# Kernel tuning notes

Hardware: AMD Instinct MI355X
Metric: run time of the kernel (lower is better)

Reference implementation:

```python
import jax, jax.numpy as jnp
import numpy as np

T = 16777216  # series length (2**24)


def setup_inputs() -> dict:
    key = jax.random.key(0)
    k1, k2 = jax.random.split(key)
    timeseries = jax.random.normal(k1, (T,), dtype=jnp.float32)
    # learned smoothing parameter alpha in (0, 1), per min_max_norm(0, 1) constraint
    alpha = jax.random.uniform(k2, (1,), dtype=jnp.float32)
    return {"timeseries": timeseries, "alpha": alpha}


def reference(timeseries, alpha):
    """Simple exponential smoothing (component form).

    level_0 = y_0; level_t = (1-alpha)*level_{t-1} + alpha*y_t for t >= 1.
    prediction_t (the forecast emitted at step t) is the level BEFORE the
    update, so the output is levels[0 : T-1], length T-1 (matches the
    original loop that emits one forecast per timestep in timeseries[1:]).

    Expressed as a first-order linear recurrence s_t = a_t * s_{t-1} + b_t
    and solved with an associative (parallel) scan.
    """
    a0 = alpha[0]
    n = timeseries.shape[0]
    dt = timeseries.dtype
    # a_0 = 0, b_0 = y_0 pins level_0 = y_0 regardless of the dummy carry.
    a = jnp.concatenate([jnp.zeros((1,), dt),
                         jnp.full((n - 1,), 1.0, dt) * (1.0 - a0)])
    b = jnp.concatenate([timeseries[:1], a0 * timeseries[1:]])

    def combine(e1, e2):
        a1, b1 = e1
        a2, b2 = e2
        return (a1 * a2, a2 * b1 + b2)

    _, levels = jax.lax.associative_scan(combine, (a, b))  # levels[t] = level_t
    return levels[:-1]
```

## Files before the change

kernel.cpp:

```cpp
#include <hip/hip_runtime.h>
#include <stdint.h>


#define BLOCK 256
#define SEG   32
#define VPT   (SEG / 4)
#define CHUNK (BLOCK * SEG)
#define NF4   (CHUNK / 4)
#define HALO  4096
#define HSEG  (HALO / BLOCK)
#define HVPT  (HSEG / 4)
#define DECAY_THR 1e-8f

typedef float f32x4 __attribute__((ext_vector_type(4)));

__device__ __forceinline__ void nt_store4(float* p, float x, float y, float z, float w) {
    f32x4 v = {x, y, z, w};
    __builtin_nontemporal_store(v, (f32x4*)p);
}

__device__ __forceinline__ int sw(int j) { return j ^ ((j >> 3) & 7); }

__device__ __forceinline__ float pow2k(float x, int k) {
    float p = x;
#pragma unroll
    for (int i = 0; i < k; ++i) p *= p;
    return p;
}

__device__ __forceinline__ void wave_scan_affine(float& a, float& b) {
    const int lane = threadIdx.x & 63;
#pragma unroll
    for (int off = 1; off < 64; off <<= 1) {
        float pa = __shfl_up(a, off);
        float pb = __shfl_up(b, off);
        if (lane >= off) {
            b = fmaf(a, pb, b);
            a = pa * a;
        }
    }
}

__device__ __forceinline__ void block_exscan_affine(
    float a, float b, float* wa, float* wb, int t, float& ea, float& eb)
{
    float ia = a, ib = b;
    wave_scan_affine(ia, ib);
    const int w = t >> 6, lane = t & 63;
    if (lane == 63) { wa[w] = ia; wb[w] = ib; }
    float xa = __shfl_up(ia, 1);
    float xb = __shfl_up(ib, 1);
    if (lane == 0) { xa = 1.0f; xb = 0.0f; }
    __syncthreads();
    float pa = 1.0f, pb = 0.0f;
#pragma unroll
    for (int i = 0; i < 3; ++i) {
        if (i < w) {
            float ca = wa[i], cb = wb[i];
            pb = fmaf(ca, pb, cb);
            pa *= ca;
        }
    }
    eb = fmaf(xa, pb, xb);
    ea = pa * xa;
}

__global__ __launch_bounds__(BLOCK) void k_block_agg(
    const float* __restrict__ y, const float* __restrict__ alpha_p,
    float* __restrict__ aggA, float* __restrict__ aggB, long n)
{
    const float alpha = alpha_p[0];
    const float oma = 1.0f - alpha;
    if (pow2k(oma, 12) < DECAY_THR) return;

    const int t = threadIdx.x;
    const long base = (long)blockIdx.x * CHUNK + (long)t * SEG;

    float a = 1.0f, s = 0.0f;
    if (base + SEG <= n) {
        const float4* p = (const float4*)(y + base);
#pragma unroll
        for (int v = 0; v < VPT; ++v) {
            float4 q = p[v];
            s = fmaf(oma, s, alpha * q.x);
            s = fmaf(oma, s, alpha * q.y);
            s = fmaf(oma, s, alpha * q.z);
            s = fmaf(oma, s, alpha * q.w);
        }
        a = pow2k(oma, 5);
    } else {
        for (int k = 0; k < SEG; ++k) {
            long idx = base + k;
            if (idx < n) { s = fmaf(oma, s, alpha * y[idx]); a *= oma; }
        }
    }

    __shared__ float wa[4], wb[4];
    wave_scan_affine(a, s);
    if ((t & 63) == 63) { wa[t >> 6] = a; wb[t >> 6] = s; }
    __syncthreads();
    if (t == 0) {
        float ta = 1.0f, tb = 0.0f;
#pragma unroll
        for (int i = 0; i < 4; ++i) {
            float ca = wa[i], cb = wb[i];
            tb = fmaf(ca, tb, cb);
            ta *= ca;
        }
        aggA[blockIdx.x] = ta;
        aggB[blockIdx.x] = tb;
    }
}

__global__ __launch_bounds__(BLOCK, 4) void k_emit(
    const float* __restrict__ y, const float* __restrict__ alpha_p,
    const float* __restrict__ aggA, const float* __restrict__ aggB,
    float* __restrict__ out, long n, int G)
{
    __shared__ float4 buf[NF4];
    __shared__ float wa[4], wb[4];
    __shared__ float s_carry;

    const int t = threadIdx.x;
    int tile = blockIdx.x;
    if ((G & 7) == 0) tile = (tile & 7) * (G >> 3) + (tile >> 3);

    const float alpha = alpha_p[0];
    const float oma   = 1.0f - alpha;
    const bool  fast  = (pow2k(oma, 12) < DECAY_THR);
    const long tbase = (long)tile * CHUNK;
    const long base  = tbase + (long)t * SEG;
    const bool fullTile = (tbase + CHUNK <= n);
    const float y0 = y[0];

    const bool do_halo = fast && (tile > 0);
    float4 hq[HVPT];
    if (do_halo) {
        const float4* hp = (const float4*)(y + (tbase - HALO)) + t * HVPT;
#pragma unroll
        for (int v = 0; v < HVPT; ++v) hq[v] = hp[v];
    }

    if (fullTile) {
        const float4* p4 = (const float4*)(y + tbase);
        float4 tmp[8];
#pragma unroll
        for (int k = 0; k < 8; ++k) tmp[k] = p4[t + (k << 8)];
#pragma unroll
        for (int k = 0; k < 8; ++k) buf[sw(t + (k << 8))] = tmp[k];
    }

    float carry = y0;
    if (do_halo) {
        float hs = 0.0f;
#pragma unroll
        for (int v = 0; v < HVPT; ++v) {
            float4 q = hq[v];
            hs = fmaf(oma, hs, alpha * q.x);
            hs = fmaf(oma, hs, alpha * q.y);
            hs = fmaf(oma, hs, alpha * q.z);
            hs = fmaf(oma, hs, alpha * q.w);
        }
        float ha = pow2k(oma, 4);
        wave_scan_affine(ha, hs);
        if ((t & 63) == 63) { wa[t >> 6] = ha; wb[t >> 6] = hs; }
        __syncthreads();
        float cb_ = 0.0f;
#pragma unroll
        for (int i = 0; i < 4; ++i) cb_ = fmaf(wa[i], cb_, wb[i]);
        carry = cb_;
    }

    __syncthreads();

    float a_seg, b_seg;
    if (fullTile) {
        float s = 0.0f;
#pragma unroll
        for (int v = 0; v < VPT; ++v) {
            float4 q = buf[sw(t * VPT + v)];
            s = fmaf(oma, s, alpha * q.x);
            s = fmaf(oma, s, alpha * q.y);
            s = fmaf(oma, s, alpha * q.z);
            s = fmaf(oma, s, alpha * q.w);
        }
        b_seg = s;
        a_seg = pow2k(oma, 5);
    } else {
        float a = 1.0f, s = 0.0f;
        for (int k = 0; k < SEG; ++k) {
            long idx = base + k;
            if (idx < n) { s = fmaf(oma, s, alpha * y[idx]); a *= oma; }
        }
        a_seg = a; b_seg = s;
    }

    float ea_th, eb_th;
    block_exscan_affine(a_seg, b_seg, wa, wb, t, ea_th, eb_th);

    if (!fast) {
        const int items = (G + BLOCK - 1) / BLOCK;
        float ta = 1.0f, tb = 0.0f;
        for (int j = 0; j < items; ++j) {
            int g = t * items + j;
            if (g < G) {
                float ca = aggA[g], cb = aggB[g];
                tb = fmaf(ca, tb, cb);
                ta *= ca;
            }
        }
        __syncthreads();
        float pa, pb;
        block_exscan_affine(ta, tb, wa, wb, t, pa, pb);
        const int q = tile / items;
        if (t == q) {
            float ea = pa, eb = pb;
            const int r = tile - q * items;
            for (int j = 0; j < r; ++j) {
                int g = q * items + j;
                float ca = aggA[g], cb = aggB[g];
                eb = fmaf(ca, eb, cb);
                ea *= ca;
            }
            s_carry = fmaf(ea, y0, eb);
        }
        __syncthreads();
        carry = s_carry;
    }

    float lvl = fmaf(ea_th, carry, eb_th);

    if (fullTile) {
#pragma unroll
        for (int v = 0; v < VPT; ++v) {
            const int pj = sw(t * VPT + v);
            float4 q = buf[pj], r;
            lvl = fmaf(oma, lvl, alpha * q.x); r.x = lvl;
            lvl = fmaf(oma, lvl, alpha * q.y); r.y = lvl;
            lvl = fmaf(oma, lvl, alpha * q.z); r.z = lvl;
            lvl = fmaf(oma, lvl, alpha * q.w); r.w = lvl;
            buf[pj] = r;
        }
        __syncthreads();
        const bool lastGuard = (tbase + CHUNK > n - 1);
#pragma unroll
        for (int k = 0; k < 8; ++k) {
            const int j = t + (k << 8);
            float4 r = buf[sw(j)];
            const long gi = tbase + 4L * j;
            if (!lastGuard) {
                nt_store4(out + gi, r.x, r.y, r.z, r.w);
            } else {
                if (gi + 4 <= n - 1) {
                    nt_store4(out + gi, r.x, r.y, r.z, r.w);
                } else {
                    if (gi + 0 < n - 1) out[gi + 0] = r.x;
                    if (gi + 1 < n - 1) out[gi + 1] = r.y;
                    if (gi + 2 < n - 1) out[gi + 2] = r.z;
                    if (gi + 3 < n - 1) out[gi + 3] = r.w;
                }
            }
        }
    } else {
        for (int k = 0; k < SEG; ++k) {
            long idx = base + k;
            if (idx < n) {
                lvl = fmaf(oma, lvl, alpha * y[idx]);
                if (idx < n - 1) out[idx] = lvl;
            }
        }
    }
}

extern "C" void kernel_launch(void* const* d_in, const int* in_sizes, int n_in,
                              void* d_out, int out_size, void* d_ws, size_t ws_size,
                              hipStream_t stream) {
    const float* y     = (const float*)d_in[0];
    const float* alpha = (const float*)d_in[1];
    float* out = (float*)d_out;
    const long n = (long)in_sizes[0];
    const int  G = (int)((n + CHUNK - 1) / CHUNK);

    float* aggA = (float*)d_ws;
    float* aggB = aggA + G;

    k_block_agg<<<G, BLOCK, 0, stream>>>(y, alpha, aggA, aggB, n);
    k_emit<<<G, BLOCK, 0, stream>>>(y, alpha, aggA, aggB, out, n, G);
}
```

Before: 113.5 us.

## Halve tile size, shrink halo, and load segments straight into registers

Result: slower. 172.0 us (+51.5%).

```diff
diff --git a/kernel.cpp b/kernel.cpp
--- a/kernel.cpp
+++ b/kernel.cpp
@@ -3,13 +3,11 @@
 
 
 #define BLOCK 256
-#define SEG   32
+#define SEG   16
 #define VPT   (SEG / 4)
 #define CHUNK (BLOCK * SEG)
 #define NF4   (CHUNK / 4)
-#define HALO  4096
-#define HSEG  (HALO / BLOCK)
-#define HVPT  (HSEG / 4)
+#define HALO  1024
 #define DECAY_THR 1e-8f
 
 typedef float f32x4 __attribute__((ext_vector_type(4)));
@@ -71,7 +69,7 @@
 {
     const float alpha = alpha_p[0];
     const float oma = 1.0f - alpha;
-    if (pow2k(oma, 12) < DECAY_THR) return;
+    if (pow2k(oma, 10) < DECAY_THR) return;
 
     const int t = threadIdx.x;
     const long base = (long)blockIdx.x * CHUNK + (long)t * SEG;
@@ -87,7 +85,7 @@
             s = fmaf(oma, s, alpha * q.z);
             s = fmaf(oma, s, alpha * q.w);
         }
-        a = pow2k(oma, 5);
+        a = pow2k(oma, 4);
     } else {
         for (int k = 0; k < SEG; ++k) {
             long idx = base + k;
@@ -112,13 +110,14 @@
     }
 }
 
-__global__ __launch_bounds__(BLOCK, 4) void k_emit(
+__global__ __launch_bounds__(BLOCK, 8) void k_emit(
     const float* __restrict__ y, const float* __restrict__ alpha_p,
     const float* __restrict__ aggA, const float* __restrict__ aggB,
     float* __restrict__ out, long n, int G)
 {
     __shared__ float4 buf[NF4];
     __shared__ float wa[4], wb[4];
+    __shared__ float hwa[4], hwb[4];
     __shared__ float s_carry;
 
     const int t = threadIdx.x;
@@ -127,65 +126,48 @@
 
     const float alpha = alpha_p[0];
     const float oma   = 1.0f - alpha;
-    const bool  fast  = (pow2k(oma, 12) < DECAY_THR);
+    const bool  fast  = (pow2k(oma, 10) < DECAY_THR);
     const long tbase = (long)tile * CHUNK;
     const long base  = tbase + (long)t * SEG;
     const bool fullTile = (tbase + CHUNK <= n);
     const float y0 = y[0];
 
     const bool do_halo = fast && (tile > 0);
-    float4 hq[HVPT];
+    float4 hq;
     if (do_halo) {
-        const float4* hp = (const float4*)(y + (tbase - HALO)) + t * HVPT;
-#pragma unroll
-        for (int v = 0; v < HVPT; ++v) hq[v] = hp[v];
-    }
-
+        hq = ((const float4*)(y + (tbase - HALO)))[t];
+    }
+
+    float4 arr[VPT];
     if (fullTile) {
-        const float4* p4 = (const float4*)(y + tbase);
-        float4 tmp[8];
-#pragma unroll
-        for (int k = 0; k < 8; ++k) tmp[k] = p4[t + (k << 8)];
-#pragma unroll
-        for (int k = 0; k < 8; ++k) buf[sw(t + (k << 8))] = tmp[k];
-    }
-
-    float carry = y0;
+        const float4* p = (const float4*)(y + base);
+#pragma unroll
+        for (int v = 0; v < VPT; ++v) arr[v] = p[v];
+    }
+
     if (do_halo) {
         float hs = 0.0f;
-#pragma unroll
-        for (int v = 0; v < HVPT; ++v) {
-            float4 q = hq[v];
-            hs = fmaf(oma, hs, alpha * q.x);
-            hs = fmaf(oma, hs, alpha * q.y);
-            hs = fmaf(oma, hs, alpha * q.z);
-            hs = fmaf(oma, hs, alpha * q.w);
-        }
-        float ha = pow2k(oma, 4);
+        hs = fmaf(oma, hs, alpha * hq.x);
+        hs = fmaf(oma, hs, alpha * hq.y);
+        hs = fmaf(oma, hs, alpha * hq.z);
+        hs = fmaf(oma, hs, alpha * hq.w);
+        float ha = pow2k(oma, 2);
         wave_scan_affine(ha, hs);
-        if ((t & 63) == 63) { wa[t >> 6] = ha; wb[t >> 6] = hs; }
-        __syncthreads();
-        float cb_ = 0.0f;
-#pragma unroll
-        for (int i = 0; i < 4; ++i) cb_ = fmaf(wa[i], cb_, wb[i]);
-        carry = cb_;
-    }
-
-    __syncthreads();
+        if ((t & 63) == 63) { hwa[t >> 6] = ha; hwb[t >> 6] = hs; }
+    }
 
     float a_seg, b_seg;
     if (fullTile) {
         float s = 0.0f;
 #pragma unroll
         for (int v = 0; v < VPT; ++v) {
-            float4 q = buf[sw(t * VPT + v)];
-            s = fmaf(oma, s, alpha * q.x);
-            s = fmaf(oma, s, alpha * q.y);
-            s = fmaf(oma, s, alpha * q.z);
-            s = fmaf(oma, s, alpha * q.w);
+            s = fmaf(oma, s, alpha * arr[v].x);
+            s = fmaf(oma, s, alpha * arr[v].y);
+            s = fmaf(oma, s, alpha * arr[v].z);
+            s = fmaf(oma, s, alpha * arr[v].w);
         }
         b_seg = s;
-        a_seg = pow2k(oma, 5);
+        a_seg = pow2k(oma, 4);
     } else {
         float a = 1.0f, s = 0.0f;
         for (int k = 0; k < SEG; ++k) {
@@ -197,6 +179,14 @@
 
     float ea_th, eb_th;
     block_exscan_affine(a_seg, b_seg, wa, wb, t, ea_th, eb_th);
+
+    float carry = y0;
+    if (do_halo) {
+        float cb_ = 0.0f;
+#pragma unroll
+        for (int i = 0; i < 4; ++i) cb_ = fmaf(hwa[i], cb_, hwb[i]);
+        carry = cb_;
+    }
 
     if (!fast) {
         const int items = (G + BLOCK - 1) / BLOCK;
@@ -233,18 +223,17 @@
     if (fullTile) {
 #pragma unroll
         for (int v = 0; v < VPT; ++v) {
-            const int pj = sw(t * VPT + v);
-            float4 q = buf[pj], r;
+            float4 q = arr[v], r;
             lvl = fmaf(oma, lvl, alpha * q.x); r.x = lvl;
             lvl = fmaf(oma, lvl, alpha * q.y); r.y = lvl;
             lvl = fmaf(oma, lvl, alpha * q.z); r.z = lvl;
             lvl = fmaf(oma, lvl, alpha * q.w); r.w = lvl;
-            buf[pj] = r;
+            buf[sw(t * VPT + v)] = r;
         }
         __syncthreads();
         const bool lastGuard = (tbase + CHUNK > n - 1);
 #pragma unroll
-        for (int k = 0; k < 8; ++k) {
+        for (int k = 0; k < 4; ++k) {
             const int j = t + (k << 8);
             float4 r = buf[sw(j)];
             const long gi = tbase + 4L * j;
```
